# Performance work log

Measured on AMD Instinct MI355X. Metric: run time of the kernel, lower is better.

The kernel has to match this reference:

```python
import jax, jax.numpy as jnp
import numpy as np

NUM_CLASSES = 2
THRESHOLD = 0.5
NEGPOS_RATIO = 3
VAR0, VAR1 = 0.1, 0.2  # self.variance = [0.1, 0.2]


def point_form(priors):
    # [cx,cy,w,h] -> [xmin,ymin,xmax,ymax]
    return jnp.concatenate([priors[:, :2] - priors[:, 2:] / 2,
                            priors[:, :2] + priors[:, 2:] / 2], axis=1)


def jaccard(a, b):
    # a: [O,4], b: [P,4] point-form -> IoU [O,P]
    tl = jnp.maximum(a[:, None, :2], b[None, :, :2])
    br = jnp.minimum(a[:, None, 2:], b[None, :, 2:])
    wh = jnp.clip(br - tl, 0.0)
    inter = wh[..., 0] * wh[..., 1]
    area_a = ((a[:, 2] - a[:, 0]) * (a[:, 3] - a[:, 1]))[:, None]
    area_b = ((b[:, 2] - b[:, 0]) * (b[:, 3] - b[:, 1]))[None, :]
    return inter / (area_a + area_b - inter)


def encode(matched, priors):
    # matched: [P,4] point-form GT, priors: [P,4] center-size
    g_cxcy = ((matched[:, :2] + matched[:, 2:]) / 2 - priors[:, :2]) / (VAR0 * priors[:, 2:])
    g_wh = jnp.log((matched[:, 2:] - matched[:, :2]) / priors[:, 2:]) / VAR1
    return jnp.concatenate([g_cxcy, g_wh], axis=1)


def match_one(truths, labels, priors):
    # truths: [O,4], labels: [O], priors: [P,4]
    O = truths.shape[0]
    overlaps = jaccard(truths, point_form(priors))          # [O,P]
    best_prior_idx = jnp.argmax(overlaps, axis=1)           # [O] best prior per GT
    best_truth_overlap = jnp.max(overlaps, axis=0)          # [P]
    best_truth_idx = jnp.argmax(overlaps, axis=0)           # [P]
    # ensure each GT keeps its best prior
    best_truth_overlap = best_truth_overlap.at[best_prior_idx].set(2.0)
    best_truth_idx = best_truth_idx.at[best_prior_idx].set(jnp.arange(O))
    matches = truths[best_truth_idx]                        # [P,4]
    conf = labels[best_truth_idx].astype(jnp.int32)         # head label == 1
    conf = jnp.where(best_truth_overlap < THRESHOLD, 0, conf)
    loc = encode(matches, priors)                           # [P,4]
    return loc, conf


def setup_inputs() -> dict:
    key = jax.random.key(0)
    k1, k2, k3, k4, k5, k6 = jax.random.split(key, 6)
    B, P, O = 32, 32768, 32
    loc_data = jax.random.normal(k1, (B, P, 3), jnp.float32) * 0.1
    conf_data = jax.random.normal(k2, (B, P, 2), jnp.float32)
    cxy = jax.random.uniform(k3, (P, 2), jnp.float32, 0.1, 0.9)
    wh = jax.random.uniform(k4, (P, 2), jnp.float32, 0.05, 0.2)
    priors = jnp.concatenate([cxy, wh], axis=1)
    xy1 = jax.random.uniform(k5, (B, O, 2), jnp.float32, 0.0, 0.7)
    twh = jax.random.uniform(k6, (B, O, 2), jnp.float32, 0.05, 0.25)
    targets = jnp.concatenate([xy1, xy1 + twh, jnp.ones((B, O, 1), jnp.float32)], axis=2)
    return {"loc_data": loc_data, "conf_data": conf_data, "priors": priors, "targets": targets}


def reference(loc_data, conf_data, priors, targets):
    B, P, _ = loc_data.shape
    # convert_coord: [cx, cy, gw] -> [cx, cy, gw, gw]
    quard = jnp.stack([loc_data[..., 0], loc_data[..., 1],
                       loc_data[..., 2], loc_data[..., 2]], axis=-1)  # [B,P,4]
    truths = targets[..., :4]
    labels = targets[..., 4]
    loc_t, conf_t = jax.vmap(lambda t, l: match_one(t, l, priors))(truths, labels)
    pos = conf_t > 0                                         # [B,P]
    # localization smooth-L1 over positives (sum reduction)
    d = quard - loc_t
    ad = jnp.abs(d)
    sl1 = jnp.where(ad < 1.0, 0.5 * d * d, ad - 0.5)
    loss_l = jnp.sum(sl1 * pos[..., None].astype(sl1.dtype))
    # per-prior CE for hard-negative mining
    lse = jax.nn.logsumexp(conf_data, axis=-1)               # [B,P]
    picked = jnp.take_along_axis(conf_data, conf_t[..., None], axis=-1)[..., 0]
    ce = lse - picked                                        # [B,P]
    ce_mine = jnp.where(pos, 0.0, ce)
    # double argsort -> rank of each prior by mining loss (descending)
    loss_idx = jnp.argsort(-ce_mine, axis=1)
    idx_rank = jnp.argsort(loss_idx, axis=1)
    num_pos = jnp.sum(pos.astype(jnp.int32), axis=1, keepdims=True)  # [B,1]
    num_neg = jnp.minimum(NEGPOS_RATIO * num_pos, P - 1)
    neg = idx_rank < num_neg
    sel = jnp.logical_or(pos, neg)
    loss_c = jnp.sum(jnp.where(sel, ce, 0.0))
    N = jnp.sum(num_pos).astype(loss_l.dtype)
    return loss_l / N, loss_c / N
```

## Files before the change

kernel.cpp:

```cpp
#include <hip/hip_runtime.h>
#include <math.h>

#define Bn 32
#define Pn 32768
#define On 32
#define TPB 256
#define PPT 4
#define BP  (TPB * PPT)
#define NCHUNK (Pn / BP)


__device__ __forceinline__ unsigned long long shfl_down_u64(unsigned long long v, int off) {
    unsigned lo = (unsigned)(v & 0xFFFFFFFFull);
    unsigned hi = (unsigned)(v >> 32);
    lo = __shfl_down(lo, off, 64);
    hi = __shfl_down(hi, off, 64);
    return ((unsigned long long)hi << 32) | lo;
}

__global__ __launch_bounds__(256) void match(const float* __restrict__ loc,
                                             const float2* __restrict__ conf2,
                                             const float4* __restrict__ priors,
                                             const float* __restrict__ targets,
                                             unsigned long long* __restrict__ bpm,
                                             float* __restrict__ ce_mine,
                                             int* __restrict__ num_pos,
                                             float* __restrict__ loss_l_t,
                                             float* __restrict__ ce_t,
                                             int* __restrict__ np_tot) {
    int b = blockIdx.y;
    int base = blockIdx.x * BP;
    int tid = threadIdx.x;
    int lane = tid & 63, wv = tid >> 6;

    __shared__ float4 tb[On];
    __shared__ float  ta[On], lb[On];
    __shared__ float  sred[12];

    if (tid < On) {
        const float* t = targets + ((size_t)b * On + tid) * 5;
        float x1 = t[0], y1 = t[1], x2 = t[2], y2 = t[3];
        tb[tid] = make_float4(x1, y1, x2, y2);
        ta[tid] = (x2 - x1) * (y2 - y1);
        lb[tid] = t[4];
    }
    __syncthreads();

    if (blockIdx.z == 0) {
        float bI[8], bU[8];
        int   bp[8];
#pragma unroll
        for (int t = 0; t < 8; t++) { bI[t] = 0.f; bU[t] = 1.f; bp[t] = base + lane; }

#pragma unroll
        for (int h = 0; h < 2; h++) {
            float ax1[8], ay1[8], ax2[8], ay2[8], aa[8];
#pragma unroll
            for (int i = 0; i < 8; i++) {
                float4 pr = priors[base + lane + 64 * (h * 8 + i)];
                ax1[i] = pr.x - pr.z * 0.5f; ay1[i] = pr.y - pr.w * 0.5f;
                ax2[i] = pr.x + pr.z * 0.5f; ay2[i] = pr.y + pr.w * 0.5f;
                aa[i]  = (ax2[i] - ax1[i]) * (ay2[i] - ay1[i]);
            }
#pragma unroll
            for (int t = 0; t < 8; t++) {
                int o = wv * 8 + t;
                float4 tt = tb[o];
                float  a  = ta[o];
#pragma unroll
                for (int i = 0; i < 8; i++) {
                    float ix1 = fmaxf(tt.x, ax1[i]), iy1 = fmaxf(tt.y, ay1[i]);
                    float ix2 = fminf(tt.z, ax2[i]), iy2 = fminf(tt.w, ay2[i]);
                    float iw = fmaxf(ix2 - ix1, 0.f), ih = fmaxf(iy2 - iy1, 0.f);
                    float I = iw * ih;
                    float U = a + aa[i] - I;
                    if (I * bU[t] > bI[t] * U) {
                        bI[t] = I; bU[t] = U; bp[t] = base + lane + 64 * (h * 8 + i);
                    }
                }
            }
        }
        unsigned long long key[8];
#pragma unroll
        for (int t = 0; t < 8; t++) {
            float iou = bI[t] / bU[t];
            key[t] = ((unsigned long long)__float_as_uint(iou) << 32)
                   | (unsigned)(Pn - 1 - bp[t]);
        }
#pragma unroll
        for (int off = 32; off > 0; off >>= 1) {
            unsigned long long other[8];
#pragma unroll
            for (int t = 0; t < 8; t++) other[t] = shfl_down_u64(key[t], off);
#pragma unroll
            for (int t = 0; t < 8; t++) if (other[t] > key[t]) key[t] = other[t];
        }
        if (lane == 0) {
#pragma unroll
            for (int t = 0; t < 8; t++)
                atomicMax(&bpm[b * On + wv * 8 + t], key[t]);
        }
        return;
    }

    float2 cc[PPT];
#pragma unroll
    for (int j = 0; j < PPT; j++) cc[j] = conf2[(size_t)b * Pn + base + tid + 256 * j];

    float px1[PPT], py1[PPT], px2[PPT], py2[PPT], ab[PPT], pcx[PPT], pcy[PPT], pw[PPT], ph[PPT];
#pragma unroll
    for (int j = 0; j < PPT; j++) {
        float4 pr = priors[base + tid + 256 * j];
        pcx[j] = pr.x; pcy[j] = pr.y; pw[j] = pr.z; ph[j] = pr.w;
        px1[j] = pr.x - pr.z * 0.5f; py1[j] = pr.y - pr.w * 0.5f;
        px2[j] = pr.x + pr.z * 0.5f; py2[j] = pr.y + pr.w * 0.5f;
        ab[j]  = (px2[j] - px1[j]) * (py2[j] - py1[j]);
    }

    float bIc[PPT][2], bUc[PPT][2];
    int   bxc[PPT][2];
#pragma unroll
    for (int j = 0; j < PPT; j++)
#pragma unroll
        for (int h = 0; h < 2; h++) { bIc[j][h] = 0.f; bUc[j][h] = 1.f; bxc[j][h] = h * 16; }

#pragma unroll 2
    for (int o16 = 0; o16 < 16; o16++) {
#pragma unroll
        for (int h = 0; h < 2; h++) {
            int o = h * 16 + o16;
            float4 tt = tb[o];
            float  a  = ta[o];
#pragma unroll
            for (int j = 0; j < PPT; j++) {
                float ix1 = fmaxf(tt.x, px1[j]), iy1 = fmaxf(tt.y, py1[j]);
                float ix2 = fminf(tt.z, px2[j]), iy2 = fminf(tt.w, py2[j]);
                float iw = fmaxf(ix2 - ix1, 0.f), ih = fmaxf(iy2 - iy1, 0.f);
                float I = iw * ih;
                float U = a + ab[j] - I;
                if (I * bUc[j][h] > bIc[j][h] * U) { bIc[j][h] = I; bUc[j][h] = U; bxc[j][h] = o; }
            }
        }
    }
    float bI[PPT], bU[PPT];
    int   bx[PPT];
#pragma unroll
    for (int j = 0; j < PPT; j++) {
        bI[j] = bIc[j][0]; bU[j] = bUc[j][0]; bx[j] = bxc[j][0];
        if (bIc[j][1] * bU[j] > bI[j] * bUc[j][1]) { bI[j] = bIc[j][1]; bU[j] = bUc[j][1]; bx[j] = bxc[j][1]; }
    }

    float ll_s = 0.f, pce_s = 0.f, cnt_s = 0.f;
#pragma unroll
    for (int j = 0; j < PPT; j++) {
        int p = base + tid + 256 * j;
        int bidx = bx[j];
        int cf = (bI[j] >= 0.5f * bU[j]) ? (int)lb[bidx] : 0;
        bool pos = cf > 0;

        if (pos) {
            float4 tt = tb[bidx];
            float g0 = ((tt.x + tt.z) * 0.5f - pcx[j]) / (0.1f * pw[j]);
            float g1 = ((tt.y + tt.w) * 0.5f - pcy[j]) / (0.1f * ph[j]);
            float g2 = __logf((tt.z - tt.x) / pw[j]) * 5.0f;
            float g3 = __logf((tt.w - tt.y) / ph[j]) * 5.0f;
            const float* lp = loc + ((size_t)b * Pn + p) * 3;
            float q0 = lp[0], q1 = lp[1], q2 = lp[2];
            float dd[4] = { q0 - g0, q1 - g1, q2 - g2, q2 - g3 };
#pragma unroll
            for (int i = 0; i < 4; i++) {
                float ad = fabsf(dd[i]);
                ll_s += (ad < 1.f) ? 0.5f * dd[i] * dd[i] : (ad - 0.5f);
            }
            cnt_s += 1.f;
        }

        float m = fmaxf(cc[j].x, cc[j].y);
        float lse = m + __logf(__expf(cc[j].x - m) + __expf(cc[j].y - m));
        float ce = lse - (cf ? cc[j].y : cc[j].x);
        if (pos) { pce_s += ce; ce = 0.f; }
        ce_mine[(size_t)b * Pn + p] = fmaxf(ce, 0.f);
    }

#pragma unroll
    for (int off = 32; off > 0; off >>= 1) {
        ll_s  += __shfl_down(ll_s,  off, 64);
        pce_s += __shfl_down(pce_s, off, 64);
        cnt_s += __shfl_down(cnt_s, off, 64);
    }
    if (lane == 0) { sred[wv * 3] = ll_s; sred[wv * 3 + 1] = pce_s; sred[wv * 3 + 2] = cnt_s; }
    __syncthreads();
    if (tid == 0) {
        float llr = 0, pcer = 0, cntr = 0;
        for (int w = 0; w < 4; w++) { llr += sred[w*3]; pcer += sred[w*3+1]; cntr += sred[w*3+2]; }
        if (llr != 0.f)  atomicAdd(loss_l_t, llr);
        if (pcer != 0.f) atomicAdd(ce_t, pcer);
        int c = (int)cntr;
        if (c) { atomicAdd(&num_pos[b], c); atomicAdd(np_tot, c); }
    }
}

__global__ __launch_bounds__(1024) void topk(const float* __restrict__ loc,
                                             const float2* __restrict__ conf2,
                                             const float4* __restrict__ priors,
                                             const float* __restrict__ targets,
                                             const unsigned long long* __restrict__ bpm,
                                             float* __restrict__ ce_mine,
                                             int* __restrict__ num_pos,
                                             float* __restrict__ ce_t,
                                             float* __restrict__ loss_l_t,
                                             int* __restrict__ np_tot,
                                             unsigned* __restrict__ tick,
                                             float* __restrict__ out) {
    int b = blockIdx.x, tid = threadIdx.x;
    int lane = tid & 63, wv = tid >> 6;

    __shared__ int hist[8192];
    __shared__ float4 ftb[On];
    __shared__ float  fta[On], flb[On];
    __shared__ int    fpr[On];
    __shared__ int    s_k;
    __shared__ unsigned s_lo;
    __shared__ int s_ab;
    __shared__ float ssum[16];
    __shared__ int   scnt[16];

    if (tid < On) {
        const float* t = targets + ((size_t)b * On + tid) * 5;
        float x1 = t[0], y1 = t[1], x2 = t[2], y2 = t[3];
        ftb[tid] = make_float4(x1, y1, x2, y2);
        fta[tid] = (x2 - x1) * (y2 - y1);
        flb[tid] = t[4];
        fpr[tid] = Pn - 1 - (int)(bpm[b * On + tid] & 0xFFFFFFFFull);
    }
    __syncthreads();
    if (tid < On) {
        int pt = fpr[tid];
        bool winner = true;
        for (int t2 = tid + 1; t2 < On; t2++) if (fpr[t2] == pt) winner = false;
        if (winner) {
            float4 pr = priors[pt];
            float pcx = pr.x, pcy = pr.y, pw = pr.z, ph = pr.w;
            float px1 = pr.x - pr.z * 0.5f, py1 = pr.y - pr.w * 0.5f;
            float px2 = pr.x + pr.z * 0.5f, py2 = pr.y + pr.w * 0.5f;
            float ab  = (px2 - px1) * (py2 - py1);
            float bIc[2] = {0.f, 0.f}, bUc[2] = {1.f, 1.f};
            int   bxc[2] = {0, 16};
            for (int o16 = 0; o16 < 16; o16++) {
                for (int h = 0; h < 2; h++) {
                    int o = h * 16 + o16;
                    float4 tt = ftb[o];
                    float  a  = fta[o];
                    float ix1 = fmaxf(tt.x, px1), iy1 = fmaxf(tt.y, py1);
                    float ix2 = fminf(tt.z, px2), iy2 = fminf(tt.w, py2);
                    float iw = fmaxf(ix2 - ix1, 0.f), ih = fmaxf(iy2 - iy1, 0.f);
                    float I = iw * ih;
                    float U = a + ab - I;
                    if (I * bUc[h] > bIc[h] * U) { bIc[h] = I; bUc[h] = U; bxc[h] = o; }
                }
            }
            float bI = bIc[0], bU = bUc[0]; int bx = bxc[0];
            if (bIc[1] * bU > bI * bUc[1]) { bI = bIc[1]; bU = bUc[1]; bx = bxc[1]; }

            int  cf_old  = (bI >= 0.5f * bU) ? (int)flb[bx] : 0;
            bool pos_old = cf_old > 0;
            int  cf_new  = (int)flb[tid];
            bool pos_new = cf_new > 0;

            float2 cc = conf2[(size_t)b * Pn + pt];
            float m = fmaxf(cc.x, cc.y);
            float lse = m + __logf(__expf(cc.x - m) + __expf(cc.y - m));
            float ce_old = lse - (cf_old ? cc.y : cc.x);
            float ce_new = lse - (cf_new ? cc.y : cc.x);

            const float* lp = loc + ((size_t)b * Pn + pt) * 3;
            float q0 = lp[0], q1 = lp[1], q2 = lp[2];
            float ll_old = 0.f, ll_new = 0.f;
            if (pos_old) {
                float4 tt = ftb[bx];
                float g0 = ((tt.x + tt.z) * 0.5f - pcx) / (0.1f * pw);
                float g1 = ((tt.y + tt.w) * 0.5f - pcy) / (0.1f * ph);
                float g2 = __logf((tt.z - tt.x) / pw) * 5.0f;
                float g3 = __logf((tt.w - tt.y) / ph) * 5.0f;
                float dd[4] = { q0 - g0, q1 - g1, q2 - g2, q2 - g3 };
                for (int i = 0; i < 4; i++) {
                    float ad = fabsf(dd[i]);
                    ll_old += (ad < 1.f) ? 0.5f * dd[i] * dd[i] : (ad - 0.5f);
                }
            }
            if (pos_new) {
                float4 tt = ftb[tid];
                float g0 = ((tt.x + tt.z) * 0.5f - pcx) / (0.1f * pw);
                float g1 = ((tt.y + tt.w) * 0.5f - pcy) / (0.1f * ph);
                float g2 = __logf((tt.z - tt.x) / pw) * 5.0f;
                float g3 = __logf((tt.w - tt.y) / ph) * 5.0f;
                float dd[4] = { q0 - g0, q1 - g1, q2 - g2, q2 - g3 };
                for (int i = 0; i < 4; i++) {
                    float ad = fabsf(dd[i]);
                    ll_new += (ad < 1.f) ? 0.5f * dd[i] * dd[i] : (ad - 0.5f);
                }
            }
            float dll = ll_new - ll_old;
            float dce = (pos_new ? ce_new : 0.f) - (pos_old ? ce_old : 0.f);
            int   dnp = (pos_new ? 1 : 0) - (pos_old ? 1 : 0);
            if (dll != 0.f) atomicAdd(loss_l_t, dll);
            if (dce != 0.f) atomicAdd(ce_t, dce);
            if (dnp) { atomicAdd(&num_pos[b], dnp); atomicAdd(np_tot, dnp); }
            float cm_new = pos_new ? 0.f : fmaxf(ce_new, 0.f);
            ce_mine[(size_t)b * Pn + pt] = cm_new;
        }
    }
    if (tid == 0) s_k = atomicAdd(&num_pos[b], 0);
    __syncthreads();

    const float4* v4 = (const float4*)(ce_mine + (size_t)b * Pn);
    float4 r[8];
#pragma unroll
    for (int i = 0; i < 8; i++) r[i] = v4[i * 1024 + tid];

    int k = 3 * s_k;
    if (k > Pn - 1) k = Pn - 1;

    if (k > 0) {
        unsigned LO = 0u;
        int AB = 0;

        const int SH[3] = {22, 11, 0};
        const int NB[3] = {512, 2048, 2048};

#pragma unroll
        for (int rd = 0; rd < 3; rd++) {
            int shift = SH[rd], nb = NB[rd];
#pragma unroll
            for (int i = 0; i < 8; i++) hist[tid + 1024 * i] = 0;
            __syncthreads();
            int* myh = hist + ((wv >> 2) << 11);
#pragma unroll
            for (int i = 0; i < 8; i++) {
                float4 rv = r[i];
                float vals[4] = {rv.x, rv.y, rv.z, rv.w};
#pragma unroll
                for (int q = 0; q < 4; q++) {
                    unsigned u = __float_as_uint(vals[q]);
                    unsigned bin = (u - LO) >> shift;
                    if (bin < (unsigned)nb) atomicAdd(&myh[bin], 1);
                }
            }
            __syncthreads();
            if (wv == 0) {
                int bpl = nb >> 6;
                int bb = lane * bpl;
                int lsum = 0;
                for (int q = 0; q < bpl; q++) {
                    int bin = bb + q;
                    lsum += hist[bin] + hist[2048 + bin] + hist[4096 + bin] + hist[6144 + bin];
                }
                int suf = lsum;
#pragma unroll
                for (int off = 1; off < 64; off <<= 1) {
                    int o = __shfl(suf, (lane + off) & 63, 64);
                    suf += ((lane + off) < 64) ? o : 0;
                }
                int kk = k - AB;
                if (suf >= kk && (suf - lsum) < kk) {
                    int acc = suf - lsum;
                    for (int q = bpl - 1; q >= 0; q--) {
                        int bin = bb + q;
                        int hc = hist[bin] + hist[2048 + bin] + hist[4096 + bin] + hist[6144 + bin];
                        acc += hc;
                        if (acc >= kk) {
                            s_lo = LO + ((unsigned)bin << shift);
                            s_ab = AB + (acc - hc);
                            break;
                        }
                    }
                }
            }
            __syncthreads();
            LO = s_lo; AB = s_ab;
        }
        float tau = __uint_as_float(LO);
        float s = 0.f; int c = 0;
#pragma unroll
        for (int i = 0; i < 8; i++) {
            if (r[i].x > tau) { s += r[i].x; c++; }
            if (r[i].y > tau) { s += r[i].y; c++; }
            if (r[i].z > tau) { s += r[i].z; c++; }
            if (r[i].w > tau) { s += r[i].w; c++; }
        }
#pragma unroll
        for (int off = 32; off > 0; off >>= 1) {
            s += __shfl_down(s, off, 64);
            c += __shfl_down(c, off, 64);
        }
        if (lane == 0) { ssum[wv] = s; scnt[wv] = c; }
        __syncthreads();
        if (tid == 0) {
            float st = 0.f; int ct = 0;
            for (int w = 0; w < 16; w++) { st += ssum[w]; ct += scnt[w]; }
            atomicAdd(ce_t, st + (float)(k - ct) * tau);
        }
    }

    if (tid == 0) {
        __threadfence();
        unsigned done = atomicAdd(tick, 1u);
        if (done == (unsigned)(Bn - 1)) {
            float N  = (float)atomicAdd(np_tot, 0);
            float ll = atomicAdd(loss_l_t, 0.f);
            float ce = atomicAdd(ce_t, 0.f);
            out[0] = ll / N;
            out[1] = ce / N;
        }
    }
}

extern "C" void kernel_launch(void* const* d_in, const int* in_sizes, int n_in,
                              void* d_out, int out_size, void* d_ws, size_t ws_size,
                              hipStream_t stream) {
    const float* loc     = (const float*)d_in[0];
    const float* conf    = (const float*)d_in[1];
    const float* priors  = (const float*)d_in[2];
    const float* targets = (const float*)d_in[3];
    float* out = (float*)d_out;

    char* ws = (char*)d_ws;
    unsigned long long* bpm = (unsigned long long*)ws;
    int*   num_pos  = (int*)(ws + 8192);
    float* loss_l_t = (float*)(ws + 8320);
    float* ce_t     = (float*)(ws + 8324);
    int*   np_tot   = (int*)(ws + 8328);
    unsigned* tick  = (unsigned*)(ws + 8332);
    float* ce_mine  = (float*)(ws + 16384);

    hipMemsetAsync(ws, 0, 16384, stream);

    hipLaunchKernelGGL(match, dim3(NCHUNK, Bn, 2), dim3(256), 0, stream,
                       loc, (const float2*)conf, (const float4*)priors, targets,
                       bpm, ce_mine, num_pos, loss_l_t, ce_t, np_tot);
    hipLaunchKernelGGL(topk, dim3(Bn), dim3(1024), 0, stream,
                       loc, (const float2*)conf, (const float4*)priors, targets, bpm,
                       ce_mine, num_pos, ce_t, loss_l_t, np_tot, tick, out);
}
```

Before: 158.6 us.

## Split per-batch top-k radix select across eight cooperating blocks

The hard-negative top-k stage now runs 8 blocks per batch, 256 in total, instead of one 1024-thread block per batch. Each block holds a 4096-element slice of ce_mine in registers. The blocks merge local radix histograms into global histograms that the match kernel zero-fills, and they synchronise through atomic spin barriers at each radix round. The goal is to use many more CUs during the selection, which was limited to 32 blocks. In exchange it adds global atomics and spin-waits that depend on all 8 blocks of a batch being resident at the same time. The old single-block path is kept as a fallback when the workspace is too small.

```diff
diff --git a/kernel.cpp b/kernel.cpp
--- a/kernel.cpp
+++ b/kernel.cpp
@@ -9,6 +9,9 @@
 #define BP  (TPB * PPT)
 #define NCHUNK (Pn / BP)
 
+
+#define HIST_OFF (16384 + 4 * Bn * Pn)
+#define HIST_BYTES (3 * Bn * 2048 * 4)
 
 __device__ __forceinline__ unsigned long long shfl_down_u64(unsigned long long v, int off) {
     unsigned lo = (unsigned)(v & 0xFFFFFFFFull);
@@ -27,11 +30,18 @@
                                              int* __restrict__ num_pos,
                                              float* __restrict__ loss_l_t,
                                              float* __restrict__ ce_t,
-                                             int* __restrict__ np_tot) {
+                                             int* __restrict__ np_tot,
+                                             int* __restrict__ ghz,
+                                             int use8) {
     int b = blockIdx.y;
     int base = blockIdx.x * BP;
     int tid = threadIdx.x;
     int lane = tid & 63, wv = tid >> 6;
+
+    if (use8) {
+        int bid = (blockIdx.z * Bn + blockIdx.y) * NCHUNK + blockIdx.x;
+        if (tid < 96) ghz[bid * 96 + tid] = 0;
+    }
 
     __shared__ float4 tb[On];
     __shared__ float  ta[On], lb[On];
@@ -200,18 +210,278 @@
     }
 }
 
-__global__ __launch_bounds__(1024) void topk(const float* __restrict__ loc,
-                                             const float2* __restrict__ conf2,
-                                             const float4* __restrict__ priors,
-                                             const float* __restrict__ targets,
-                                             const unsigned long long* __restrict__ bpm,
-                                             float* __restrict__ ce_mine,
-                                             int* __restrict__ num_pos,
-                                             float* __restrict__ ce_t,
-                                             float* __restrict__ loss_l_t,
-                                             int* __restrict__ np_tot,
-                                             unsigned* __restrict__ tick,
-                                             float* __restrict__ out) {
+__device__ __forceinline__ float fixup_delta(int tidx, int pt,
+                                             const float4* ftb, const float* fta, const float* flb,
+                                             const float* loc, const float2* conf2,
+                                             const float4* priors, int b,
+                                             float* loss_l_t, float* ce_t,
+                                             int* num_pos, int* np_tot) {
+    float4 pr = priors[pt];
+    float pcx = pr.x, pcy = pr.y, pw = pr.z, ph = pr.w;
+    float px1 = pr.x - pr.z * 0.5f, py1 = pr.y - pr.w * 0.5f;
+    float px2 = pr.x + pr.z * 0.5f, py2 = pr.y + pr.w * 0.5f;
+    float ab  = (px2 - px1) * (py2 - py1);
+    float bIc[2] = {0.f, 0.f}, bUc[2] = {1.f, 1.f};
+    int   bxc[2] = {0, 16};
+    for (int o16 = 0; o16 < 16; o16++) {
+        for (int h = 0; h < 2; h++) {
+            int o = h * 16 + o16;
+            float4 tt = ftb[o];
+            float  a  = fta[o];
+            float ix1 = fmaxf(tt.x, px1), iy1 = fmaxf(tt.y, py1);
+            float ix2 = fminf(tt.z, px2), iy2 = fminf(tt.w, py2);
+            float iw = fmaxf(ix2 - ix1, 0.f), ih = fmaxf(iy2 - iy1, 0.f);
+            float I = iw * ih;
+            float U = a + ab - I;
+            if (I * bUc[h] > bIc[h] * U) { bIc[h] = I; bUc[h] = U; bxc[h] = o; }
+        }
+    }
+    float bI = bIc[0], bU = bUc[0]; int bx = bxc[0];
+    if (bIc[1] * bU > bI * bUc[1]) { bI = bIc[1]; bU = bUc[1]; bx = bxc[1]; }
+
+    int  cf_old  = (bI >= 0.5f * bU) ? (int)flb[bx] : 0;
+    bool pos_old = cf_old > 0;
+    int  cf_new  = (int)flb[tidx];
+    bool pos_new = cf_new > 0;
+
+    float2 cc = conf2[(size_t)b * Pn + pt];
+    float m = fmaxf(cc.x, cc.y);
+    float lse = m + __logf(__expf(cc.x - m) + __expf(cc.y - m));
+    float ce_old = lse - (cf_old ? cc.y : cc.x);
+    float ce_new = lse - (cf_new ? cc.y : cc.x);
+
+    const float* lp = loc + ((size_t)b * Pn + pt) * 3;
+    float q0 = lp[0], q1 = lp[1], q2 = lp[2];
+    float ll_old = 0.f, ll_new = 0.f;
+    if (pos_old) {
+        float4 tt = ftb[bx];
+        float g0 = ((tt.x + tt.z) * 0.5f - pcx) / (0.1f * pw);
+        float g1 = ((tt.y + tt.w) * 0.5f - pcy) / (0.1f * ph);
+        float g2 = __logf((tt.z - tt.x) / pw) * 5.0f;
+        float g3 = __logf((tt.w - tt.y) / ph) * 5.0f;
+        float dd[4] = { q0 - g0, q1 - g1, q2 - g2, q2 - g3 };
+        for (int i = 0; i < 4; i++) {
+            float ad = fabsf(dd[i]);
+            ll_old += (ad < 1.f) ? 0.5f * dd[i] * dd[i] : (ad - 0.5f);
+        }
+    }
+    if (pos_new) {
+        float4 tt = ftb[tidx];
+        float g0 = ((tt.x + tt.z) * 0.5f - pcx) / (0.1f * pw);
+        float g1 = ((tt.y + tt.w) * 0.5f - pcy) / (0.1f * ph);
+        float g2 = __logf((tt.z - tt.x) / pw) * 5.0f;
+        float g3 = __logf((tt.w - tt.y) / ph) * 5.0f;
+        float dd[4] = { q0 - g0, q1 - g1, q2 - g2, q2 - g3 };
+        for (int i = 0; i < 4; i++) {
+            float ad = fabsf(dd[i]);
+            ll_new += (ad < 1.f) ? 0.5f * dd[i] * dd[i] : (ad - 0.5f);
+        }
+    }
+    float dll = ll_new - ll_old;
+    float dce = (pos_new ? ce_new : 0.f) - (pos_old ? ce_old : 0.f);
+    int   dnp = (pos_new ? 1 : 0) - (pos_old ? 1 : 0);
+    if (dll != 0.f) atomicAdd(loss_l_t, dll);
+    if (dce != 0.f) atomicAdd(ce_t, dce);
+    if (dnp) { atomicAdd(&num_pos[b], dnp); atomicAdd(np_tot, dnp); }
+    return pos_new ? 0.f : fmaxf(ce_new, 0.f);
+}
+
+__global__ __launch_bounds__(1024) void topk8(const float* __restrict__ loc,
+                                              const float2* __restrict__ conf2,
+                                              const float4* __restrict__ priors,
+                                              const float* __restrict__ targets,
+                                              const unsigned long long* __restrict__ bpm,
+                                              const float* __restrict__ ce_mine,
+                                              int* __restrict__ num_pos,
+                                              float* __restrict__ ce_t,
+                                              float* __restrict__ loss_l_t,
+                                              int* __restrict__ np_tot,
+                                              unsigned* __restrict__ tick,
+                                              unsigned* __restrict__ rcnt,
+                                              int* __restrict__ gcnt,
+                                              int* __restrict__ gh,
+                                              float* __restrict__ out) {
+    int x = blockIdx.x, b = blockIdx.y, tid = threadIdx.x;
+    int lane = tid & 63, wv = tid >> 6;
+
+    __shared__ int hist[2048];
+    __shared__ float4 ftb[On];
+    __shared__ float  fta[On], flb[On];
+    __shared__ int    fpr[On];
+    __shared__ int    sfp[On];
+    __shared__ float  sfv[On];
+    __shared__ int s_k;
+    __shared__ unsigned s_lo;
+    __shared__ int s_ab;
+    __shared__ float ssum[16];
+    __shared__ int   scnt[16];
+
+    const float4* v4 = (const float4*)(ce_mine + (size_t)b * Pn + (size_t)x * 4096);
+    float4 r = v4[tid];
+
+    if (tid < On) {
+        const float* t = targets + ((size_t)b * On + tid) * 5;
+        float x1 = t[0], y1 = t[1], x2 = t[2], y2 = t[3];
+        ftb[tid] = make_float4(x1, y1, x2, y2);
+        fta[tid] = (x2 - x1) * (y2 - y1);
+        flb[tid] = t[4];
+        fpr[tid] = Pn - 1 - (int)(bpm[b * On + tid] & 0xFFFFFFFFull);
+        sfp[tid] = -1;
+    }
+    __syncthreads();
+    if (tid < On) {
+        int pt = fpr[tid];
+        bool winner = true;
+        for (int t2 = tid + 1; t2 < On; t2++) if (fpr[t2] == pt) winner = false;
+        if (winner && (pt >> 12) == x) {
+            float cm_new = fixup_delta(tid, pt, ftb, fta, flb, loc, conf2, priors, b,
+                                       loss_l_t, ce_t, num_pos, np_tot);
+            sfp[tid] = pt & 4095;
+            sfv[tid] = cm_new;
+        }
+    }
+    __syncthreads();
+    for (int t = 0; t < On; t++) {
+        int lp2 = sfp[t];
+        if (lp2 >= 0 && (lp2 >> 2) == tid) {
+            float v = sfv[t];
+            int c = lp2 & 3;
+            if (c == 0) r.x = v; else if (c == 1) r.y = v;
+            else if (c == 2) r.z = v; else r.w = v;
+        }
+    }
+    __syncthreads();
+    if (tid == 0) {
+        atomicAdd(&rcnt[b * 5 + 0], 1u);
+        while (atomicAdd(&rcnt[b * 5 + 0], 0u) < 8u) __builtin_amdgcn_s_sleep(8);
+        s_k = 3 * atomicAdd(&num_pos[b], 0);
+    }
+    __syncthreads();
+    int k = s_k;
+    if (k > Pn - 1) k = Pn - 1;
+
+    unsigned LO = 0u;
+    int AB = 0;
+    float tau = 0.f;
+
+    if (k > 0) {
+        const int SH[3] = {20, 9, 0};
+        const int NB[3] = {2048, 2048, 512};
+        int* gh_b;
+#pragma unroll
+        for (int rd = 0; rd < 3; rd++) {
+            int shift = SH[rd], nb = NB[rd];
+            gh_b = gh + (rd * Bn + b) * 2048;
+            hist[tid] = 0; hist[tid + 1024] = 0;
+            __syncthreads();
+            {
+                float vals[4] = {r.x, r.y, r.z, r.w};
+#pragma unroll
+                for (int q = 0; q < 4; q++) {
+                    unsigned u = __float_as_uint(vals[q]);
+                    unsigned bin = (u - LO) >> shift;
+                    if (bin < (unsigned)nb) atomicAdd(&hist[bin], 1);
+                }
+            }
+            __syncthreads();
+            int h0 = hist[2 * tid], h1 = hist[2 * tid + 1];
+            if (h0) atomicAdd(&gh_b[2 * tid], h0);
+            if (h1) atomicAdd(&gh_b[2 * tid + 1], h1);
+            __syncthreads();
+            if (tid == 0) {
+                atomicAdd(&rcnt[b * 5 + 1 + rd], 1u);
+                while (atomicAdd(&rcnt[b * 5 + 1 + rd], 0u) < 8u) __builtin_amdgcn_s_sleep(8);
+            }
+            __syncthreads();
+            if (wv == 0) {
+                int ch[32];
+                int lsum = 0;
+#pragma unroll
+                for (int q = 0; q < 32; q++) {
+                    int c = atomicAdd(&gh_b[lane * 32 + q], 0);
+                    ch[q] = c; lsum += c;
+                }
+                int suf = lsum;
+#pragma unroll
+                for (int off = 1; off < 64; off <<= 1) {
+                    int o = __shfl(suf, (lane + off) & 63, 64);
+                    suf += ((lane + off) < 64) ? o : 0;
+                }
+                int kk = k - AB;
+                if (suf >= kk && (suf - lsum) < kk) {
+                    int acc = suf - lsum;
+                    int done = 0;
+#pragma unroll
+                    for (int q = 31; q >= 0; q--) {
+                        if (!done) {
+                            acc += ch[q];
+                            if (acc >= kk) {
+                                s_lo = LO + ((unsigned)(lane * 32 + q) << shift);
+                                s_ab = AB + (acc - ch[q]);
+                                done = 1;
+                            }
+                        }
+                    }
+                }
+            }
+            __syncthreads();
+            LO = s_lo; AB = s_ab;
+        }
+        tau = __uint_as_float(LO);
+        float s = 0.f; int c = 0;
+        if (r.x > tau) { s += r.x; c++; }
+        if (r.y > tau) { s += r.y; c++; }
+        if (r.z > tau) { s += r.z; c++; }
+        if (r.w > tau) { s += r.w; c++; }
+#pragma unroll
+        for (int off = 32; off > 0; off >>= 1) {
+            s += __shfl_down(s, off, 64);
+            c += __shfl_down(c, off, 64);
+        }
+        if (lane == 0) { ssum[wv] = s; scnt[wv] = c; }
+        __syncthreads();
+        if (tid == 0) {
+            float st = 0.f; int ct = 0;
+            for (int w = 0; w < 16; w++) { st += ssum[w]; ct += scnt[w]; }
+            if (st != 0.f) atomicAdd(ce_t, st);
+            if (ct)        atomicAdd(&gcnt[b], ct);
+        }
+    }
+
+    __syncthreads();
+    if (tid == 0) {
+        unsigned done = atomicAdd(&rcnt[b * 5 + 4], 1u);
+        if (done == 7u) {
+            if (k > 0) {
+                int ct = atomicAdd(&gcnt[b], 0);
+                float tie = (float)(k - ct) * tau;
+                if (tie != 0.f) atomicAdd(ce_t, tie);
+            }
+            __threadfence();
+            unsigned d2 = atomicAdd(tick, 1u);
+            if (d2 == (unsigned)(Bn - 1)) {
+                float N  = (float)atomicAdd(np_tot, 0);
+                float ll = atomicAdd(loss_l_t, 0.f);
+                float ce = atomicAdd(ce_t, 0.f);
+                out[0] = ll / N;
+                out[1] = ce / N;
+            }
+        }
+    }
+}
+
+__global__ __launch_bounds__(1024) void topk1(const float* __restrict__ loc,
+                                              const float2* __restrict__ conf2,
+                                              const float4* __restrict__ priors,
+                                              const float* __restrict__ targets,
+                                              const unsigned long long* __restrict__ bpm,
+                                              float* __restrict__ ce_mine,
+                                              int* __restrict__ num_pos,
+                                              float* __restrict__ ce_t,
+                                              float* __restrict__ loss_l_t,
+                                              int* __restrict__ np_tot,
+                                              unsigned* __restrict__ tick,
+                                              float* __restrict__ out) {
     int b = blockIdx.x, tid = threadIdx.x;
     int lane = tid & 63, wv = tid >> 6;
 
@@ -239,74 +509,8 @@
         bool winner = true;
         for (int t2 = tid + 1; t2 < On; t2++) if (fpr[t2] == pt) winner = false;
         if (winner) {
-            float4 pr = priors[pt];
-            float pcx = pr.x, pcy = pr.y, pw = pr.z, ph = pr.w;
-            float px1 = pr.x - pr.z * 0.5f, py1 = pr.y - pr.w * 0.5f;
-            float px2 = pr.x + pr.z * 0.5f, py2 = pr.y + pr.w * 0.5f;
-            float ab  = (px2 - px1) * (py2 - py1);
-            float bIc[2] = {0.f, 0.f}, bUc[2] = {1.f, 1.f};
-            int   bxc[2] = {0, 16};
-            for (int o16 = 0; o16 < 16; o16++) {
-                for (int h = 0; h < 2; h++) {
-                    int o = h * 16 + o16;
-                    float4 tt = ftb[o];
-                    float  a  = fta[o];
-                    float ix1 = fmaxf(tt.x, px1), iy1 = fmaxf(tt.y, py1);
-                    float ix2 = fminf(tt.z, px2), iy2 = fminf(tt.w, py2);
-                    float iw = fmaxf(ix2 - ix1, 0.f), ih = fmaxf(iy2 - iy1, 0.f);
-                    float I = iw * ih;
-                    float U = a + ab - I;
-                    if (I * bUc[h] > bIc[h] * U) { bIc[h] = I; bUc[h] = U; bxc[h] = o; }
-                }
-            }
-            float bI = bIc[0], bU = bUc[0]; int bx = bxc[0];
-            if (bIc[1] * bU > bI * bUc[1]) { bI = bIc[1]; bU = bUc[1]; bx = bxc[1]; }
-
-            int  cf_old  = (bI >= 0.5f * bU) ? (int)flb[bx] : 0;
-            bool pos_old = cf_old > 0;
-            int  cf_new  = (int)flb[tid];
-            bool pos_new = cf_new > 0;
-
-            float2 cc = conf2[(size_t)b * Pn + pt];
-            float m = fmaxf(cc.x, cc.y);
-            float lse = m + __logf(__expf(cc.x - m) + __expf(cc.y - m));
-            float ce_old = lse - (cf_old ? cc.y : cc.x);
-            float ce_new = lse - (cf_new ? cc.y : cc.x);
-
-            const float* lp = loc + ((size_t)b * Pn + pt) * 3;
-            float q0 = lp[0], q1 = lp[1], q2 = lp[2];
-            float ll_old = 0.f, ll_new = 0.f;
-            if (pos_old) {
-                float4 tt = ftb[bx];
-                float g0 = ((tt.x + tt.z) * 0.5f - pcx) / (0.1f * pw);
-                float g1 = ((tt.y + tt.w) * 0.5f - pcy) / (0.1f * ph);
-                float g2 = __logf((tt.z - tt.x) / pw) * 5.0f;
-                float g3 = __logf((tt.w - tt.y) / ph) * 5.0f;
-                float dd[4] = { q0 - g0, q1 - g1, q2 - g2, q2 - g3 };
-                for (int i = 0; i < 4; i++) {
-                    float ad = fabsf(dd[i]);
-                    ll_old += (ad < 1.f) ? 0.5f * dd[i] * dd[i] : (ad - 0.5f);
-                }
-            }
-            if (pos_new) {
-                float4 tt = ftb[tid];
-                float g0 = ((tt.x + tt.z) * 0.5f - pcx) / (0.1f * pw);
-                float g1 = ((tt.y + tt.w) * 0.5f - pcy) / (0.1f * ph);
-                float g2 = __logf((tt.z - tt.x) / pw) * 5.0f;
-                float g3 = __logf((tt.w - tt.y) / ph) * 5.0f;
-                float dd[4] = { q0 - g0, q1 - g1, q2 - g2, q2 - g3 };
-                for (int i = 0; i < 4; i++) {
-                    float ad = fabsf(dd[i]);
-                    ll_new += (ad < 1.f) ? 0.5f * dd[i] * dd[i] : (ad - 0.5f);
-                }
-            }
-            float dll = ll_new - ll_old;
-            float dce = (pos_new ? ce_new : 0.f) - (pos_old ? ce_old : 0.f);
-            int   dnp = (pos_new ? 1 : 0) - (pos_old ? 1 : 0);
-            if (dll != 0.f) atomicAdd(loss_l_t, dll);
-            if (dce != 0.f) atomicAdd(ce_t, dce);
-            if (dnp) { atomicAdd(&num_pos[b], dnp); atomicAdd(np_tot, dnp); }
-            float cm_new = pos_new ? 0.f : fmaxf(ce_new, 0.f);
+            float cm_new = fixup_delta(tid, pt, ftb, fta, flb, loc, conf2, priors, b,
+                                       loss_l_t, ce_t, num_pos, np_tot);
             ce_mine[(size_t)b * Pn + pt] = cm_new;
         }
     }
@@ -324,7 +528,6 @@
     if (k > 0) {
         unsigned LO = 0u;
         int AB = 0;
-
         const int SH[3] = {22, 11, 0};
         const int NB[3] = {512, 2048, 2048};
 
@@ -431,14 +634,25 @@
     float* ce_t     = (float*)(ws + 8324);
     int*   np_tot   = (int*)(ws + 8328);
     unsigned* tick  = (unsigned*)(ws + 8332);
+    unsigned* rcnt  = (unsigned*)(ws + 8464);
+    int*   gcnt     = (int*)(ws + 9104);
     float* ce_mine  = (float*)(ws + 16384);
+    int*   gh       = (int*)(ws + HIST_OFF);
+
+    int use8 = (ws_size >= (size_t)HIST_OFF + HIST_BYTES) ? 1 : 0;
 
     hipMemsetAsync(ws, 0, 16384, stream);
 
     hipLaunchKernelGGL(match, dim3(NCHUNK, Bn, 2), dim3(256), 0, stream,
                        loc, (const float2*)conf, (const float4*)priors, targets,
-                       bpm, ce_mine, num_pos, loss_l_t, ce_t, np_tot);
-    hipLaunchKernelGGL(topk, dim3(Bn), dim3(1024), 0, stream,
-                       loc, (const float2*)conf, (const float4*)priors, targets, bpm,
-                       ce_mine, num_pos, ce_t, loss_l_t, np_tot, tick, out);
+                       bpm, ce_mine, num_pos, loss_l_t, ce_t, np_tot, gh, use8);
+    if (use8) {
+        hipLaunchKernelGGL(topk8, dim3(8, Bn), dim3(1024), 0, stream,
+                           loc, (const float2*)conf, (const float4*)priors, targets, bpm,
+                           ce_mine, num_pos, ce_t, loss_l_t, np_tot, tick, rcnt, gcnt, gh, out);
+    } else {
+        hipLaunchKernelGGL(topk1, dim3(Bn), dim3(1024), 0, stream,
+                           loc, (const float2*)conf, (const float4*)priors, targets, bpm,
+                           ce_mine, num_pos, ce_t, loss_l_t, np_tot, tick, out);
+    }
 }
```

After: 163.5 us. 3.1% more time.
